# Performance work log

Measured on AMD Instinct MI355X. Metric: run time of the kernel, lower is better.

## Reference

```python
import jax, jax.numpy as jnp
import numpy as np

BN_EPS = 1e-5
ATT_EPS = 1e-6


def _conv(x, w, groups=1):
    # x: [B,C,H,W], w: [O, C//groups, k, k], stride 1, SAME padding for odd k
    k = w.shape[-1]
    p = (k - 1) // 2
    return jax.lax.conv_general_dilated(
        x, w, window_strides=(1, 1), padding=[(p, p), (p, p)],
        dimension_numbers=('NCHW', 'OIHW', 'NCHW'), feature_group_count=groups)


def _bn(x, bnp):
    # bnp: [4, C] stacked (scale, bias, running_mean, running_var); eval-mode BN
    s, b, m, v = bnp[0], bnp[1], bnp[2], bnp[3]
    inv = s / jnp.sqrt(v + BN_EPS)
    return x * inv[None, :, None, None] + (b - m * inv)[None, :, None, None]


def _relu6(x):
    return jnp.clip(x, 0.0, 6.0)


def _ffn(x, fc1_w, fc1_bn, conv1_w, conv1_bn, conv2_w, conv2_bn, fc2_w, fc2_bn):
    # E_FFN: 1x1 ConvBNReLU6 -> dw5x5 ConvBNReLU6 & dw3x3 ConvBNReLU6 -> sum -> 1x1 ConvBN -> ReLU6
    C = x.shape[1]
    h = _relu6(_bn(_conv(x, fc1_w), fc1_bn))
    x1 = _relu6(_bn(_conv(h, conv1_w, groups=C), conv1_bn))
    x2 = _relu6(_bn(_conv(h, conv2_w, groups=C), conv2_bn))
    return _relu6(_bn(_conv(x1 + x2, fc2_w), fc2_bn))


def _bias(y, b):
    return y + b[None, :, None, None]


def setup_inputs() -> dict:
    key = jax.random.key(0)
    ks = jax.random.split(key, 16)
    C, M = 64, 8  # in_places, in_places // scale
    B, H, W = 4, 224, 224

    def w(k, shape, s=0.05):
        return (jax.random.normal(k, shape, dtype=jnp.float32) * s)

    def bn_params(k, c):
        k1, k2, k3, k4 = jax.random.split(k, 4)
        scale = 1.0 + 0.1 * jax.random.normal(k1, (c,), dtype=jnp.float32)
        bias = 0.1 * jax.random.normal(k2, (c,), dtype=jnp.float32)
        mean = 0.1 * jax.random.normal(k3, (c,), dtype=jnp.float32)
        var = 1.0 + 0.1 * jax.random.uniform(k4, (c,), dtype=jnp.float32)
        return jnp.stack([scale, bias, mean, var])  # [4, c]

    return {
        'x': jax.random.normal(ks[0], (B, C, H, W), dtype=jnp.float32),
        'gamma': jnp.full((1,), 0.5, dtype=jnp.float32),  # nonzero so attention branch matters
        'q_w': w(ks[1], (M, C, 1, 1)), 'q_b': w(ks[2], (M,)),
        'k_w': w(ks[3], (M, C, 1, 1)), 'k_b': w(ks[4], (M,)),
        'v_w': w(ks[5], (C, C, 1, 1)), 'v_b': w(ks[6], (C,)),
        'fc1_w': w(ks[7], (C, C, 1, 1)), 'fc1_bn': bn_params(ks[8], C),
        'conv1_w': w(ks[9], (C, 1, 5, 5)), 'conv1_bn': bn_params(ks[10], C),
        'conv2_w': w(ks[11], (C, 1, 3, 3)), 'conv2_bn': bn_params(ks[12], C),
        'fc2_w': w(ks[13], (C, C, 1, 1)), 'fc2_bn': bn_params(ks[14], C),
    }


def reference(x, gamma, q_w, q_b, k_w, k_b, v_w, v_b,
              fc1_w, fc1_bn, conv1_w, conv1_bn, conv2_w, conv2_bn, fc2_w, fc2_bn):
    B, C, H, W = x.shape
    N = H * W
    x_channel = _ffn(x, fc1_w, fc1_bn, conv1_w, conv1_bn, conv2_w, conv2_bn, fc2_w, fc2_bn)
    # softplus feature maps; Q,K: [B, m, N]
    Q = jax.nn.softplus(_bias(_conv(x, q_w), q_b).reshape(B, -1, N))
    K = jax.nn.softplus(_bias(_conv(x, k_w), k_b).reshape(B, -1, N))
    V = (_bias(_conv(x, v_w), v_b) + x_channel).reshape(B, C, N)
    Qt = jnp.swapaxes(Q, 1, 2)                              # [B, N, m]
    KV = jnp.einsum('bmn,bcn->bmc', K, V)                   # [B, m, C]
    norm = 1.0 / jnp.einsum('bnm,bm->bn', Qt, K.sum(-1) + ATT_EPS)  # [B, N]
    wv = jnp.einsum('bnm,bmc,bn->bcn', Qt, KV, norm).reshape(B, C, H, W)
    return x + gamma * wv
```

## Files before the change

### kernel.cpp

```cpp
#include <hip/hip_runtime.h>
#include <math.h>

#define B_ 4
#define C_ 64
#define M_ 8
#define H_ 224
#define W_ 224
#define N_ (H_*W_)
#define CN_ (C_*N_)
#define MN_ (M_*N_)
#define BCN_ (B_*CN_)
#define BMN_ (B_*MN_)

typedef __attribute__((ext_vector_type(8))) short short8;
typedef __attribute__((ext_vector_type(4))) float f32x4;
typedef __attribute__((ext_vector_type(4))) unsigned int uint4v;

__device__ __forceinline__ float relu6f(float v){ return fminf(fmaxf(v,0.0f),6.0f); }
__device__ __forceinline__ float softplusf(float v){
  return v > 0.0f ? v + log1pf(expf(-v)) : log1pf(expf(v));
}
__device__ __forceinline__ unsigned int rne2(float lo, float hi){
  unsigned int ul = __float_as_uint(lo); ul += 0x7FFFu + ((ul>>16)&1u);
  unsigned int uh = __float_as_uint(hi); uh += 0x7FFFu + ((uh>>16)&1u);
  return (ul>>16) | (uh & 0xFFFF0000u);
}

__device__ __forceinline__ short8 bfrag(const unsigned short* __restrict__ L,
                                        int px, int c0){
  const unsigned short* p = L + c0*128 + px;
  unsigned int w0 = (unsigned int)p[0]   | ((unsigned int)p[128]<<16);
  unsigned int w1 = (unsigned int)p[256] | ((unsigned int)p[384]<<16);
  unsigned int w2 = (unsigned int)p[512] | ((unsigned int)p[640]<<16);
  unsigned int w3 = (unsigned int)p[768] | ((unsigned int)p[896]<<16);
  uint4v q = {w0,w1,w2,w3};
  return __builtin_bit_cast(short8, q);
}
__device__ __forceinline__ short8 afrag(const float* __restrict__ W, int idx){
  const float4 f0 = *(const float4*)(W + idx);
  const float4 f1 = *(const float4*)(W + idx + 4);
  uint4v q = {rne2(f0.x,f0.y), rne2(f0.z,f0.w), rne2(f1.x,f1.y), rne2(f1.z,f1.w)};
  return __builtin_bit_cast(short8, q);
}
__device__ __forceinline__ short8 zfrag(){
  uint4v q = {0u,0u,0u,0u};
  return __builtin_bit_cast(short8, q);
}

__global__ __launch_bounds__(256) void k_fc1k(const float* __restrict__ x,
                                              const float* __restrict__ w,
                                              const float* __restrict__ bn,
                                              const float* __restrict__ kw,
                                              const float* __restrict__ kb,
                                              float* __restrict__ h,
                                              float* __restrict__ Kq)
{
  __shared__ unsigned short xls[64*128];
  __shared__ float invb[2][64];
  const int tid  = threadIdx.x;
  const int b    = blockIdx.x / 392;
  const int pg   = blockIdx.x % 392;
  const int pix0 = pg*128;
  const float* xb = x + (size_t)b*CN_ + pix0;

  const int scp = tid >> 5;
  const int spx = (tid & 31) << 2;
  #pragma unroll
  for (int i = 0; i < 8; ++i) {
    const int c = i*8 + scp;
    const float4 xr = *(const float4*)(xb + (size_t)c*N_ + spx);
    *(uint2*)&xls[c*128 + spx] = make_uint2(rne2(xr.x,xr.y), rne2(xr.z,xr.w));
  }
  if (tid < 64) {
    const float inv = bn[tid] / sqrtf(bn[192+tid] + 1e-5f);
    invb[0][tid] = inv;
    invb[1][tid] = bn[64+tid] - bn[128+tid]*inv;
  }
  __syncthreads();

  const int lane = tid & 63, wv = tid >> 6;
  const int l15 = lane & 15, u = lane >> 4;
  const int pxw = wv*32;

  f32x4 acc[5][2];
  #pragma unroll
  for (int t = 0; t < 5; ++t)
    #pragma unroll
    for (int s2 = 0; s2 < 2; ++s2) acc[t][s2] = (f32x4){0.f,0.f,0.f,0.f};

  #pragma unroll
  for (int kk = 0; kk < 2; ++kk) {
    const int c0 = kk*32 + u*8;
    const short8 a0 = afrag(w, (0*16+l15)*64 + c0);
    const short8 a1 = afrag(w, (1*16+l15)*64 + c0);
    const short8 a2 = afrag(w, (2*16+l15)*64 + c0);
    const short8 a3 = afrag(w, (3*16+l15)*64 + c0);
    const short8 a4 = (l15 < 8) ? afrag(kw, l15*64 + c0) : zfrag();
    #pragma unroll
    for (int s2 = 0; s2 < 2; ++s2) {
      const short8 bx = bfrag(xls, pxw + s2*16 + l15, c0);
      acc[0][s2] = __builtin_amdgcn_mfma_f32_16x16x32_bf16(a0, bx, acc[0][s2], 0,0,0);
      acc[1][s2] = __builtin_amdgcn_mfma_f32_16x16x32_bf16(a1, bx, acc[1][s2], 0,0,0);
      acc[2][s2] = __builtin_amdgcn_mfma_f32_16x16x32_bf16(a2, bx, acc[2][s2], 0,0,0);
      acc[3][s2] = __builtin_amdgcn_mfma_f32_16x16x32_bf16(a3, bx, acc[3][s2], 0,0,0);
      acc[4][s2] = __builtin_amdgcn_mfma_f32_16x16x32_bf16(a4, bx, acc[4][s2], 0,0,0);
    }
  }

  float* hb = h + (size_t)b*CN_ + pix0;
  #pragma unroll
  for (int t = 0; t < 4; ++t) {
    #pragma unroll
    for (int s2 = 0; s2 < 2; ++s2) {
      const int px = pxw + s2*16 + l15;
      #pragma unroll
      for (int r = 0; r < 4; ++r) {
        const int oc = t*16 + u*4 + r;
        hb[(size_t)oc*N_ + px] = relu6f(fmaf(acc[t][s2][r], invb[0][oc], invb[1][oc]));
      }
    }
  }
  if (u < 2) {
    float* Kb = Kq + (size_t)b*MN_ + pix0;
    #pragma unroll
    for (int s2 = 0; s2 < 2; ++s2) {
      const int px = pxw + s2*16 + l15;
      #pragma unroll
      for (int r = 0; r < 4; ++r) {
        const int m = u*4 + r;
        Kb[(size_t)m*N_ + px] = softplusf(acc[4][s2][r] + kb[m]);
      }
    }
  }
}

__global__ __launch_bounds__(256) void k_dw(const float* __restrict__ h,
                                            const float* __restrict__ w5,
                                            const float* __restrict__ w3,
                                            const float* __restrict__ bn1,
                                            const float* __restrict__ bn2,
                                            float* __restrict__ s)
{
  __shared__ float tile[36*37];
  const int tid = threadIdx.x;
  const int blk = blockIdx.x;
  const int t   = blk % 49;
  const int bc  = blk / 49;
  const int c   = bc & 63;
  const int tx0 = (t % 7) * 32;
  const int ty0 = (t / 7) * 32;
  const float* hb = h + (size_t)bc * N_;

  for (int idx = tid; idx < 1296; idx += 256) {
    const int ly = idx / 36, lx = idx - ly*36;
    const int gy = ty0 + ly - 2, gx = tx0 + lx - 2;
    float v = 0.0f;
    if (gy >= 0 && gy < H_ && gx >= 0 && gx < W_) v = hb[gy*W_ + gx];
    tile[ly*37 + lx] = v;
  }
  __syncthreads();

  float w5r[25], w3r[9];
  #pragma unroll
  for (int i = 0; i < 25; ++i) w5r[i] = w5[c*25 + i];
  #pragma unroll
  for (int i = 0; i < 9; ++i)  w3r[i] = w3[c*9 + i];
  const float inv1 = bn1[c] / sqrtf(bn1[192+c] + 1e-5f);
  const float bet1 = bn1[64+c] - bn1[128+c]*inv1;
  const float inv2 = bn2[c] / sqrtf(bn2[192+c] + 1e-5f);
  const float bet2 = bn2[64+c] - bn2[128+c]*inv2;

  const int ty  = tid >> 3;
  const int tx4 = (tid & 7) << 2;
  float a5[4] = {0,0,0,0}, a3[4] = {0,0,0,0};
  #pragma unroll
  for (int dy = 0; dy < 5; ++dy) {
    float r[8];
    #pragma unroll
    for (int i = 0; i < 8; ++i) r[i] = tile[(ty+dy)*37 + tx4 + i];
    #pragma unroll
    for (int dx = 0; dx < 5; ++dx) {
      const float wv = w5r[dy*5+dx];
      #pragma unroll
      for (int p = 0; p < 4; ++p) a5[p] = fmaf(wv, r[p+dx], a5[p]);
    }
    if (dy >= 1 && dy <= 3) {
      #pragma unroll
      for (int dx = 1; dx <= 3; ++dx) {
        const float wv = w3r[(dy-1)*3+(dx-1)];
        #pragma unroll
        for (int p = 0; p < 4; ++p) a3[p] = fmaf(wv, r[p+dx], a3[p]);
      }
    }
  }
  float* sb = s + (size_t)bc * N_ + (ty0+ty)*W_ + tx0 + tx4;
  float4 o4;
  o4.x = relu6f(fmaf(a5[0],inv1,bet1)) + relu6f(fmaf(a3[0],inv2,bet2));
  o4.y = relu6f(fmaf(a5[1],inv1,bet1)) + relu6f(fmaf(a3[1],inv2,bet2));
  o4.z = relu6f(fmaf(a5[2],inv1,bet1)) + relu6f(fmaf(a3[2],inv2,bet2));
  o4.w = relu6f(fmaf(a5[3],inv1,bet1)) + relu6f(fmaf(a3[3],inv2,bet2));
  *(float4*)sb = o4;
}

__global__ __launch_bounds__(256) void k_v(const float* __restrict__ x,
                                           const float* __restrict__ s,
                                           const float* __restrict__ vw,
                                           const float* __restrict__ vb,
                                           const float* __restrict__ fw,
                                           const float* __restrict__ fbn,
                                           float* __restrict__ V)
{
  __shared__ unsigned short xls[64*128];
  __shared__ unsigned short sls[64*128];
  __shared__ float invb[3][64];
  const int tid  = threadIdx.x;
  const int b    = blockIdx.x / 392;
  const int pg   = blockIdx.x % 392;
  const int pix0 = pg*128;
  const float* xb = x + (size_t)b*CN_ + pix0;
  const float* sb = s + (size_t)b*CN_ + pix0;

  const int scp = tid >> 5;
  const int spx = (tid & 31) << 2;
  #pragma unroll
  for (int i = 0; i < 8; ++i) {
    const int c = i*8 + scp;
    const float4 xr = *(const float4*)(xb + (size_t)c*N_ + spx);
    const float4 sr = *(const float4*)(sb + (size_t)c*N_ + spx);
    *(uint2*)&xls[c*128 + spx] = make_uint2(rne2(xr.x,xr.y), rne2(xr.z,xr.w));
    *(uint2*)&sls[c*128 + spx] = make_uint2(rne2(sr.x,sr.y), rne2(sr.z,sr.w));
  }
  if (tid < 64) {
    const float inv = fbn[tid] / sqrtf(fbn[192+tid] + 1e-5f);
    invb[0][tid] = inv;
    invb[1][tid] = fbn[64+tid] - fbn[128+tid]*inv;
    invb[2][tid] = vb[tid];
  }
  __syncthreads();

  const int lane = tid & 63, wv = tid >> 6;
  const int l15 = lane & 15, u = lane >> 4;
  const int pxw = wv*32;

  f32x4 av[4][2], af[4][2];
  #pragma unroll
  for (int t = 0; t < 4; ++t)
    #pragma unroll
    for (int s2 = 0; s2 < 2; ++s2) { av[t][s2] = (f32x4){0.f,0.f,0.f,0.f};
                                     af[t][s2] = (f32x4){0.f,0.f,0.f,0.f}; }

  #pragma unroll
  for (int kk = 0; kk < 2; ++kk) {
    const int c0 = kk*32 + u*8;
    {
      const short8 a0 = afrag(vw, (0*16+l15)*64 + c0);
      const short8 a1 = afrag(vw, (1*16+l15)*64 + c0);
      const short8 a2 = afrag(vw, (2*16+l15)*64 + c0);
      const short8 a3 = afrag(vw, (3*16+l15)*64 + c0);
      #pragma unroll
      for (int s2 = 0; s2 < 2; ++s2) {
        const short8 bx = bfrag(xls, pxw + s2*16 + l15, c0);
        av[0][s2] = __builtin_amdgcn_mfma_f32_16x16x32_bf16(a0, bx, av[0][s2], 0,0,0);
        av[1][s2] = __builtin_amdgcn_mfma_f32_16x16x32_bf16(a1, bx, av[1][s2], 0,0,0);
        av[2][s2] = __builtin_amdgcn_mfma_f32_16x16x32_bf16(a2, bx, av[2][s2], 0,0,0);
        av[3][s2] = __builtin_amdgcn_mfma_f32_16x16x32_bf16(a3, bx, av[3][s2], 0,0,0);
      }
    }
    {
      const short8 a0 = afrag(fw, (0*16+l15)*64 + c0);
      const short8 a1 = afrag(fw, (1*16+l15)*64 + c0);
      const short8 a2 = afrag(fw, (2*16+l15)*64 + c0);
      const short8 a3 = afrag(fw, (3*16+l15)*64 + c0);
      #pragma unroll
      for (int s2 = 0; s2 < 2; ++s2) {
        const short8 bs = bfrag(sls, pxw + s2*16 + l15, c0);
        af[0][s2] = __builtin_amdgcn_mfma_f32_16x16x32_bf16(a0, bs, af[0][s2], 0,0,0);
        af[1][s2] = __builtin_amdgcn_mfma_f32_16x16x32_bf16(a1, bs, af[1][s2], 0,0,0);
        af[2][s2] = __builtin_amdgcn_mfma_f32_16x16x32_bf16(a2, bs, af[2][s2], 0,0,0);
        af[3][s2] = __builtin_amdgcn_mfma_f32_16x16x32_bf16(a3, bs, af[3][s2], 0,0,0);
      }
    }
  }

  float* Vb = V + (size_t)b*CN_ + pix0;
  #pragma unroll
  for (int t = 0; t < 4; ++t) {
    #pragma unroll
    for (int s2 = 0; s2 < 2; ++s2) {
      const int px = pxw + s2*16 + l15;
      #pragma unroll
      for (int r = 0; r < 4; ++r) {
        const int oc = t*16 + u*4 + r;
        Vb[(size_t)oc*N_ + px] = av[t][s2][r] + invb[2][oc]
            + relu6f(fmaf(af[t][s2][r], invb[0][oc], invb[1][oc]));
      }
    }
  }
}

__global__ __launch_bounds__(256) void k_kv(const float* __restrict__ V,
                                            const float* __restrict__ Kq,
                                            float* __restrict__ KV,
                                            float* __restrict__ Ksum)
{
  const int blk = blockIdx.x;
  const int b   = blk >> 7;
  const int rem = blk & 127;
  const int cg  = rem >> 4;
  const int ch  = rem & 15;
  const int tid = threadIdx.x;
  const int base = ch * 3136;
  const int end  = base + 3136;
  const float* Kb = Kq + (size_t)b*MN_;
  const float* Vb = V  + (size_t)b*CN_ + (size_t)(cg*8)*N_;

  float acc[64];
  #pragma unroll
  for (int i = 0; i < 64; ++i) acc[i] = 0.0f;
  float ks[8] = {0,0,0,0,0,0,0,0};

  for (int n4 = base + tid*4; n4 < end; n4 += 1024) {
    float4 kr[8];
    #pragma unroll
    for (int m2 = 0; m2 < 8; ++m2) kr[m2] = *(const float4*)(Kb + (size_t)m2*N_ + n4);
    #pragma unroll
    for (int m2 = 0; m2 < 8; ++m2)
      ks[m2] += (kr[m2].x + kr[m2].y) + (kr[m2].z + kr[m2].w);
    #pragma unroll
    for (int c8 = 0; c8 < 8; ++c8) {
      const float4 vv = *(const float4*)(Vb + (size_t)c8*N_ + n4);
      #pragma unroll
      for (int m2 = 0; m2 < 8; ++m2) {
        float t = acc[m2*8+c8];
        t = fmaf(kr[m2].x, vv.x, t);
        t = fmaf(kr[m2].y, vv.y, t);
        t = fmaf(kr[m2].z, vv.z, t);
        t = fmaf(kr[m2].w, vv.w, t);
        acc[m2*8+c8] = t;
      }
    }
  }
  const int lane = tid & 63;

  {
    int nv = 64;
    #pragma unroll
    for (int mask = 1; mask <= 32; mask <<= 1) {
      nv >>= 1;
      const bool hi = (lane & mask) != 0;
      #pragma unroll
      for (int i = 0; i < 32; ++i) {
        if (i < nv) {
          const float mine = hi ? acc[i] : acc[i+nv];
          const float th = __shfl_xor(mine, mask);
          acc[i] = (hi ? acc[i+nv] : acc[i]) + th;
        }
      }
    }
  }
  const int j = 32*(lane & 1) + 16*((lane >> 1) & 1) + 8*((lane >> 2) & 1)
              + 4*((lane >> 3) & 1) + 2*((lane >> 4) & 1) + ((lane >> 5) & 1);
  atomicAdd(&KV[b*512 + (j >> 3)*64 + cg*8 + (j & 7)], acc[0]);

  if (cg == 0) {
    float mk = 0.0f;
    #pragma unroll
    for (int jj = 0; jj < 8; ++jj) {
      float v = ks[jj];
      v += __shfl_xor(v, 1);
      v += __shfl_xor(v, 2);
      v += __shfl_xor(v, 4);
      v += __shfl_xor(v, 8);
      v += __shfl_xor(v, 16);
      v += __shfl_xor(v, 32);
      if (lane == jj) mk = v;
    }
    if (lane < 8) atomicAdd(&Ksum[b*8 + lane], mk);
  }
}

__global__ __launch_bounds__(256) void k_out(const float* __restrict__ x,
                                             const float* __restrict__ qw,
                                             const float* __restrict__ qb,
                                             const float* __restrict__ gamma,
                                             const float* __restrict__ KV,
                                             const float* __restrict__ Ksum,
                                             float* __restrict__ out)
{
  __shared__ float xs[64*128];
  __shared__ __align__(16) float kvt[64*8];
  __shared__ __align__(16) float qwt[64*8];
  __shared__ float qs[8][128];
  __shared__ float scl[128];
  __shared__ float ksl[8];
  const int tid = threadIdx.x;
  const int b  = blockIdx.x / 392;
  const int pg = blockIdx.x % 392;
  const int pix0 = pg*128;
  const float* xb = x + (size_t)b*CN_ + pix0;

  for (int idx = tid; idx < 512; idx += 256) {
    const int m = idx >> 6, c = idx & 63;
    kvt[c*8 + m] = KV[b*512 + idx];
    qwt[c*8 + m] = qw[idx];
  }
  if (tid < 8) ksl[tid] = Ksum[b*8 + tid] + 1e-6f;
  #pragma unroll
  for (int i = 0; i < 8; ++i) {
    const int idx = i*256 + tid;
    const int c = idx >> 5, p4 = (idx & 31) << 2;
    const float4 v = *(const float4*)(xb + (size_t)c*N_ + p4);
    *(float4*)&xs[c*128 + p4] = v;
  }
  __syncthreads();

  if (tid < 128) {
    const int px = tid;
    float q[8] = {0,0,0,0,0,0,0,0};
    #pragma unroll 8
    for (int c = 0; c < 64; ++c) {
      const float xv = xs[c*128 + px];
      const float4 w0 = *(const float4*)&qwt[c*8];
      const float4 w1 = *(const float4*)&qwt[c*8+4];
      q[0] = fmaf(w0.x, xv, q[0]);
      q[1] = fmaf(w0.y, xv, q[1]);
      q[2] = fmaf(w0.z, xv, q[2]);
      q[3] = fmaf(w0.w, xv, q[3]);
      q[4] = fmaf(w1.x, xv, q[4]);
      q[5] = fmaf(w1.y, xv, q[5]);
      q[6] = fmaf(w1.z, xv, q[6]);
      q[7] = fmaf(w1.w, xv, q[7]);
    }
    float den = 0.0f;
    #pragma unroll
    for (int m = 0; m < 8; ++m) {
      q[m] = softplusf(q[m] + qb[m]);
      den  = fmaf(q[m], ksl[m], den);
      qs[m][px] = q[m];
    }
    scl[px] = gamma[0] / den;
  }
  __syncthreads();

  float* ob = out + (size_t)b*CN_ + pix0;
  #pragma unroll
  for (int i = 0; i < 32; ++i) {
    const int idx = i*256 + tid;
    const int c = idx >> 7, px = idx & 127;
    const float4 k0 = *(const float4*)&kvt[c*8];
    const float4 k1 = *(const float4*)&kvt[c*8+4];
    float wv;
    wv = qs[0][px]*k0.x;
    wv = fmaf(qs[1][px], k0.y, wv);
    wv = fmaf(qs[2][px], k0.z, wv);
    wv = fmaf(qs[3][px], k0.w, wv);
    wv = fmaf(qs[4][px], k1.x, wv);
    wv = fmaf(qs[5][px], k1.y, wv);
    wv = fmaf(qs[6][px], k1.z, wv);
    wv = fmaf(qs[7][px], k1.w, wv);
    ob[(size_t)c*N_ + px] = fmaf(scl[px], wv, xs[c*128 + px]);
  }
}

extern "C" void kernel_launch(void* const* d_in, const int* in_sizes, int n_in,
                              void* d_out, int out_size, void* d_ws, size_t ws_size,
                              hipStream_t stream) {
  const float* x      = (const float*)d_in[0];
  const float* gamma  = (const float*)d_in[1];
  const float* q_w    = (const float*)d_in[2];
  const float* q_b    = (const float*)d_in[3];
  const float* k_w    = (const float*)d_in[4];
  const float* k_b    = (const float*)d_in[5];
  const float* v_w    = (const float*)d_in[6];
  const float* v_b    = (const float*)d_in[7];
  const float* fc1_w  = (const float*)d_in[8];
  const float* fc1_bn = (const float*)d_in[9];
  const float* c1_w   = (const float*)d_in[10];
  const float* c1_bn  = (const float*)d_in[11];
  const float* c2_w   = (const float*)d_in[12];
  const float* c2_bn  = (const float*)d_in[13];
  const float* fc2_w  = (const float*)d_in[14];
  const float* fc2_bn = (const float*)d_in[15];
  float* outp = (float*)d_out;

  float* ws   = (float*)d_ws;
  float* bufA = ws;
  float* bufS = ws + (size_t)BCN_;
  float* bufK = ws + (size_t)2*BCN_;
  float* kv   = ws + (size_t)2*BCN_ + BMN_;
  float* ksum = kv + 2048;

  hipMemsetAsync(kv, 0, (2048 + 32)*sizeof(float), stream);

  k_fc1k<<<dim3(B_*392), dim3(256), 0, stream>>>(x, fc1_w, fc1_bn, k_w, k_b, bufA, bufK);
  k_dw  <<<dim3(B_*C_*49), dim3(256), 0, stream>>>(bufA, c1_w, c2_w, c1_bn, c2_bn, bufS);
  k_v   <<<dim3(B_*392), dim3(256), 0, stream>>>(x, bufS, v_w, v_b, fc2_w, fc2_bn, bufA);
  k_kv  <<<dim3(512), dim3(256), 0, stream>>>(bufA, bufK, kv, ksum);
  k_out <<<dim3(B_*392), dim3(256), 0, stream>>>(x, q_w, q_b, gamma, kv, ksum, outp);
}
```

Measured before the change: 301.5 us.

## Fuse KV reduction into V kernel, replace atomics with deterministic partial reduction

```diff
diff --git a/kernel.cpp b/kernel.cpp
--- a/kernel.cpp
+++ b/kernel.cpp
@@ -11,6 +11,7 @@
 #define MN_ (M_*N_)
 #define BCN_ (B_*CN_)
 #define BMN_ (B_*MN_)
+#define NPG_ 392
 
 typedef __attribute__((ext_vector_type(8))) short short8;
 typedef __attribute__((ext_vector_type(4))) float f32x4;
@@ -58,8 +59,8 @@
   __shared__ unsigned short xls[64*128];
   __shared__ float invb[2][64];
   const int tid  = threadIdx.x;
-  const int b    = blockIdx.x / 392;
-  const int pg   = blockIdx.x % 392;
+  const int b    = blockIdx.x / NPG_;
+  const int pg   = blockIdx.x % NPG_;
   const int pix0 = pg*128;
   const float* xb = x + (size_t)b*CN_ + pix0;
 
@@ -202,20 +203,25 @@
   *(float4*)sb = o4;
 }
 
-__global__ __launch_bounds__(256) void k_v(const float* __restrict__ x,
-                                           const float* __restrict__ s,
-                                           const float* __restrict__ vw,
-                                           const float* __restrict__ vb,
-                                           const float* __restrict__ fw,
-                                           const float* __restrict__ fbn,
-                                           float* __restrict__ V)
+__global__ __launch_bounds__(256) void k_vkv(const float* __restrict__ x,
+                                             const float* __restrict__ s,
+                                             const float* __restrict__ vw,
+                                             const float* __restrict__ vb,
+                                             const float* __restrict__ fw,
+                                             const float* __restrict__ fbn,
+                                             const float* __restrict__ Kq,
+                                             float* __restrict__ kv_part,
+                                             float* __restrict__ ks_part)
 {
-  __shared__ unsigned short xls[64*128];
-  __shared__ unsigned short sls[64*128];
+  __shared__ __align__(16) unsigned char smem[32768];
+  unsigned short* xls = (unsigned short*)smem;
+  unsigned short* sls = (unsigned short*)(smem + 16384);
+  float* kvw = (float*)smem;
+  float* kl  = (float*)(smem + 16384);
   __shared__ float invb[3][64];
   const int tid  = threadIdx.x;
-  const int b    = blockIdx.x / 392;
-  const int pg   = blockIdx.x % 392;
+  const int b    = blockIdx.x / NPG_;
+  const int pg   = blockIdx.x % NPG_;
   const int pix0 = pg*128;
   const float* xb = x + (size_t)b*CN_ + pix0;
   const float* sb = s + (size_t)b*CN_ + pix0;
@@ -282,100 +288,108 @@
     }
   }
 
-  float* Vb = V + (size_t)b*CN_ + pix0;
   #pragma unroll
   for (int t = 0; t < 4; ++t) {
     #pragma unroll
     for (int s2 = 0; s2 < 2; ++s2) {
-      const int px = pxw + s2*16 + l15;
       #pragma unroll
       for (int r = 0; r < 4; ++r) {
         const int oc = t*16 + u*4 + r;
-        Vb[(size_t)oc*N_ + px] = av[t][s2][r] + invb[2][oc]
+        av[t][s2][r] = av[t][s2][r] + invb[2][oc]
             + relu6f(fmaf(af[t][s2][r], invb[0][oc], invb[1][oc]));
       }
     }
   }
-}
-
-__global__ __launch_bounds__(256) void k_kv(const float* __restrict__ V,
-                                            const float* __restrict__ Kq,
-                                            float* __restrict__ KV,
-                                            float* __restrict__ Ksum)
+  __syncthreads();
+
+  {
+    const float* Kb = Kq + (size_t)b*MN_ + pix0;
+    for (int idx = tid; idx < 1024; idx += 256)
+      kl[idx] = Kb[(size_t)(idx >> 7)*N_ + (idx & 127)];
+  }
+  __syncthreads();
+
+  {
+    const int m = tid >> 5, p0 = tid & 31;
+    float ss = kl[m*128 + p0] + kl[m*128 + p0 + 32]
+             + kl[m*128 + p0 + 64] + kl[m*128 + p0 + 96];
+    ss += __shfl_xor(ss, 1);  ss += __shfl_xor(ss, 2);
+    ss += __shfl_xor(ss, 4);  ss += __shfl_xor(ss, 8);
+    ss += __shfl_xor(ss, 16);
+    if ((tid & 31) == 0)
+      ks_part[(size_t)(b*NPG_ + pg)*8 + m] = ss;
+  }
+
+  const int jrev = 8*(l15&1) + 4*((l15>>1)&1) + 2*((l15>>2)&1) + ((l15>>3)&1);
+  const int cdst = (jrev>>2)*16 + u*4 + (jrev&3);
+  #pragma unroll
+  for (int m = 0; m < 8; ++m) {
+    const float k0 = kl[m*128 + pxw + l15];
+    const float k1 = kl[m*128 + pxw + 16 + l15];
+    float p[16];
+    #pragma unroll
+    for (int t = 0; t < 4; ++t)
+      #pragma unroll
+      for (int r = 0; r < 4; ++r)
+        p[t*4+r] = fmaf(k0, av[t][0][r], k1 * av[t][1][r]);
+    int nv = 16;
+    #pragma unroll
+    for (int mask = 1; mask <= 8; mask <<= 1) {
+      nv >>= 1;
+      const bool hi = (l15 & mask) != 0;
+      #pragma unroll
+      for (int i = 0; i < 8; ++i) {
+        if (i < nv) {
+          const float mine = hi ? p[i] : p[i+nv];
+          const float th = __shfl_xor(mine, mask);
+          p[i] = (hi ? p[i+nv] : p[i]) + th;
+        }
+      }
+    }
+    kvw[wv*512 + m*64 + cdst] = p[0];
+  }
+  __syncthreads();
+
+  float* kp = kv_part + (size_t)(b*NPG_ + pg)*512;
+  kp[tid]       = (kvw[0*512 + tid]     + kvw[1*512 + tid])
+                + (kvw[2*512 + tid]     + kvw[3*512 + tid]);
+  kp[tid + 256] = (kvw[0*512 + tid+256] + kvw[1*512 + tid+256])
+                + (kvw[2*512 + tid+256] + kvw[3*512 + tid+256]);
+}
+
+__global__ __launch_bounds__(256) void k_red(const float* __restrict__ kv_part,
+                                             const float* __restrict__ ks_part,
+                                             float* __restrict__ KV,
+                                             float* __restrict__ Ksum)
 {
+  __shared__ float red[4][64];
+  __shared__ float rks[256];
   const int blk = blockIdx.x;
-  const int b   = blk >> 7;
-  const int rem = blk & 127;
-  const int cg  = rem >> 4;
-  const int ch  = rem & 15;
-  const int tid = threadIdx.x;
-  const int base = ch * 3136;
-  const int end  = base + 3136;
-  const float* Kb = Kq + (size_t)b*MN_;
-  const float* Vb = V  + (size_t)b*CN_ + (size_t)(cg*8)*N_;
-
-  float acc[64];
-  #pragma unroll
-  for (int i = 0; i < 64; ++i) acc[i] = 0.0f;
-  float ks[8] = {0,0,0,0,0,0,0,0};
-
-  for (int n4 = base + tid*4; n4 < end; n4 += 1024) {
-    float4 kr[8];
-    #pragma unroll
-    for (int m2 = 0; m2 < 8; ++m2) kr[m2] = *(const float4*)(Kb + (size_t)m2*N_ + n4);
-    #pragma unroll
-    for (int m2 = 0; m2 < 8; ++m2)
-      ks[m2] += (kr[m2].x + kr[m2].y) + (kr[m2].z + kr[m2].w);
-    #pragma unroll
-    for (int c8 = 0; c8 < 8; ++c8) {
-      const float4 vv = *(const float4*)(Vb + (size_t)c8*N_ + n4);
-      #pragma unroll
-      for (int m2 = 0; m2 < 8; ++m2) {
-        float t = acc[m2*8+c8];
-        t = fmaf(kr[m2].x, vv.x, t);
-        t = fmaf(kr[m2].y, vv.y, t);
-        t = fmaf(kr[m2].z, vv.z, t);
-        t = fmaf(kr[m2].w, vv.w, t);
-        acc[m2*8+c8] = t;
-      }
-    }
-  }
-  const int lane = tid & 63;
-
-  {
-    int nv = 64;
-    #pragma unroll
-    for (int mask = 1; mask <= 32; mask <<= 1) {
-      nv >>= 1;
-      const bool hi = (lane & mask) != 0;
-      #pragma unroll
-      for (int i = 0; i < 32; ++i) {
-        if (i < nv) {
-          const float mine = hi ? acc[i] : acc[i+nv];
-          const float th = __shfl_xor(mine, mask);
-          acc[i] = (hi ? acc[i+nv] : acc[i]) + th;
-        }
-      }
-    }
-  }
-  const int j = 32*(lane & 1) + 16*((lane >> 1) & 1) + 8*((lane >> 2) & 1)
-              + 4*((lane >> 3) & 1) + 2*((lane >> 4) & 1) + ((lane >> 5) & 1);
-  atomicAdd(&KV[b*512 + (j >> 3)*64 + cg*8 + (j & 7)], acc[0]);
-
-  if (cg == 0) {
-    float mk = 0.0f;
-    #pragma unroll
-    for (int jj = 0; jj < 8; ++jj) {
-      float v = ks[jj];
-      v += __shfl_xor(v, 1);
-      v += __shfl_xor(v, 2);
-      v += __shfl_xor(v, 4);
-      v += __shfl_xor(v, 8);
-      v += __shfl_xor(v, 16);
-      v += __shfl_xor(v, 32);
-      if (lane == jj) mk = v;
-    }
-    if (lane < 8) atomicAdd(&Ksum[b*8 + lane], mk);
+  const int b = blk >> 3, seg = blk & 7;
+  const int t = threadIdx.x;
+  const int i = seg*64 + (t & 63);
+  const int sl = t >> 6;
+  const float* base = kv_part + (size_t)b*NPG_*512 + i;
+  float a = 0.0f;
+  for (int g = sl; g < NPG_; g += 4) a += base[(size_t)g*512];
+  red[sl][t & 63] = a;
+  __syncthreads();
+  if (t < 64)
+    KV[b*512 + seg*64 + t] = (red[0][t] + red[1][t]) + (red[2][t] + red[3][t]);
+
+  if (seg == 0) {
+    const int m = t & 7, g0 = t >> 3;
+    float s2 = 0.0f;
+    for (int g = g0; g < NPG_; g += 32)
+      s2 += ks_part[(size_t)b*NPG_*8 + g*8 + m];
+    rks[t] = s2;
+    __syncthreads();
+    if (t < 8) {
+      float s3 = 0.0f;
+      #pragma unroll
+      for (int j2 = 0; j2 < 32; ++j2) s3 += rks[j2*8 + t];
+      Ksum[b*8 + t] = s3;
+    }
   }
 }
 
@@ -394,8 +408,8 @@
   __shared__ float scl[128];
   __shared__ float ksl[8];
   const int tid = threadIdx.x;
-  const int b  = blockIdx.x / 392;
-  const int pg = blockIdx.x % 392;
+  const int b  = blockIdx.x / NPG_;
+  const int pg = blockIdx.x % NPG_;
   const int pix0 = pg*128;
   const float* xb = x + (size_t)b*CN_ + pix0;
 
@@ -483,18 +497,18 @@
   const float* fc2_bn = (const float*)d_in[15];
   float* outp = (float*)d_out;
 
-  float* ws   = (float*)d_ws;
-  float* bufA = ws;
-  float* bufS = ws + (size_t)BCN_;
-  float* bufK = ws + (size_t)2*BCN_;
-  float* kv   = ws + (size_t)2*BCN_ + BMN_;
-  float* ksum = kv + 2048;
-
-  hipMemsetAsync(kv, 0, (2048 + 32)*sizeof(float), stream);
-
-  k_fc1k<<<dim3(B_*392), dim3(256), 0, stream>>>(x, fc1_w, fc1_bn, k_w, k_b, bufA, bufK);
+  float* ws      = (float*)d_ws;
+  float* bufA    = ws;
+  float* bufS    = ws + (size_t)BCN_;
+  float* bufK    = ws + (size_t)2*BCN_;
+  float* ks_part = ws + (size_t)2*BCN_ + BMN_;
+  float* kv      = ks_part + (size_t)B_*NPG_*8;
+  float* ksum    = kv + 2048;
+  float* kv_part = bufA;
+
+  k_fc1k<<<dim3(B_*NPG_), dim3(256), 0, stream>>>(x, fc1_w, fc1_bn, k_w, k_b, bufA, bufK);
   k_dw  <<<dim3(B_*C_*49), dim3(256), 0, stream>>>(bufA, c1_w, c2_w, c1_bn, c2_bn, bufS);
-  k_v   <<<dim3(B_*392), dim3(256), 0, stream>>>(x, bufS, v_w, v_b, fc2_w, fc2_bn, bufA);
-  k_kv  <<<dim3(512), dim3(256), 0, stream>>>(bufA, bufK, kv, ksum);
-  k_out <<<dim3(B_*392), dim3(256), 0, stream>>>(x, q_w, q_b, gamma, kv, ksum, outp);
-}
+  k_vkv <<<dim3(B_*NPG_), dim3(256), 0, stream>>>(x, bufS, v_w, v_b, fc2_w, fc2_bn, bufK, kv_part, ks_part);
+  k_red <<<dim3(32), dim3(256), 0, stream>>>(kv_part, ks_part, kv, ksum);
+  k_out <<<dim3(B_*NPG_), dim3(256), 0, stream>>>(x, q_w, q_b, gamma, kv, ksum, outp);
+}
```

Result: slower. 446.0 us (+47.9%).
